# Kernel optimization log

Hardware: AMD Instinct MI355X
Metric: run time of the kernel (lower is better)

## Reference

```python
import jax, jax.numpy as jnp
import numpy as np


def _w2_1d(u, v):
    """Squared W2 distance between two 1D densities on grid positions arange(n)/n."""
    u = u / (jnp.sum(u) + 1e-10)
    v = v / (jnp.sum(v) + 1e-10)
    u_cdf = jnp.cumsum(u)                       # [n]
    v_cdf = jnp.cumsum(v)                       # [n]
    qs = jnp.sort(jnp.concatenate([u_cdf, v_cdf]))  # [2n]
    n = u.shape[0]
    pos = jnp.arange(n, dtype=u.dtype) / n      # support positions (n == m here)
    # quantile functions via searchsorted (side='left', same as torch default) + clamped gather
    u_q = pos[jnp.clip(jnp.searchsorted(u_cdf, qs), 0, n - 1)]
    v_q = pos[jnp.clip(jnp.searchsorted(v_cdf, qs), 0, n - 1)]
    delta = jnp.diff(qs, prepend=0.0)           # qs padded with leading zero, then diff
    return jnp.sum(delta * (u_q - v_q) ** 2)    # p = 2


def setup_inputs() -> dict:
    key = jax.random.key(0)
    k1, k2 = jax.random.split(key)
    B, S, T, R = 4, 8, 2048, 256
    x = jax.random.normal(k1, (B, S, T, R), dtype=jnp.float32)
    y = jax.random.normal(k2, (B, S, T, R), dtype=jnp.float32)
    return {"x": x, "y": y}


def reference(x, y):
    B, S, T, R = x.shape
    # transform_nonnegative, method='linear': shift by 1.1 * global min (if negative)
    mn = jnp.minimum(jnp.min(x), jnp.min(y))
    mn = jnp.where(mn < 0, mn, jnp.zeros((), x.dtype))
    x = x - 1.1 * mn
    y = y - 1.1 * mn
    # normalize along time axis (dim=2), sum-to-1
    x = x / jnp.sum(x, axis=2, keepdims=True)
    y = y / jnp.sum(y, axis=2, keepdims=True)
    # flatten (B, S, R) problems; each 1D distribution lives along the time axis
    xr = jnp.transpose(x, (0, 1, 3, 2)).reshape(-1, T)  # [B*S*R, T]
    yr = jnp.transpose(y, (0, 1, 3, 2)).reshape(-1, T)
    w2 = jax.vmap(_w2_1d)(xr, yr).reshape(B, S, R)
    return jnp.sum(w2, axis=(1, 2))  # loss per batch element, shape [B]
```

## Files before the change

### kernel.cpp

```cpp
#include <hip/hip_runtime.h>

#define T_N 2048
#define R_N 256
#define SLICES 32
#define NELEM (SLICES * T_N * R_N)
#define INFV 3.0e38f
#define MIN_BLOCKS 2048
#define MIN_THREADS (MIN_BLOCKS * 256)
#define LSTR 2056

#define XS(e) ((e) ^ (((e) >> 4) & 30))

#define DPPMIN(x, ctrl, rmask)                                                 \
    fminf((x), __int_as_float(__builtin_amdgcn_update_dpp(                     \
        0x7f800000, __float_as_int(x), (ctrl), (rmask), 0xf, false)))

#define DPPADDF(x, ctrl, rmask)                                                \
    x += __int_as_float(__builtin_amdgcn_update_dpp(                           \
        0, __float_as_int(x), (ctrl), (rmask), 0xf, false))

#define DPPSCAN(x)                                                             \
    do {                                                                       \
        DPPADDF(x, 0x111, 0xf);                                \
        DPPADDF(x, 0x112, 0xf);                                \
        DPPADDF(x, 0x114, 0xf);                                \
        DPPADDF(x, 0x118, 0xf);                                \
        DPPADDF(x, 0x142, 0xa);                  \
        DPPADDF(x, 0x143, 0xc);                  \
    } while (0)

__global__ __launch_bounds__(256) void kmin(const float* __restrict__ x,
                                            const float* __restrict__ y,
                                            float* __restrict__ partial,
                                            float* __restrict__ out) {
    if (blockIdx.x == 0 && threadIdx.x < 4) out[threadIdx.x] = 0.0f;
    const int g0 = blockIdx.x * 256 + threadIdx.x;
    const float4* __restrict__ x4 = (const float4*)x;
    const float4* __restrict__ y4 = (const float4*)y;
    float m0 = INFV, m1 = INFV;
    #pragma unroll
    for (int half = 0; half < 2; ++half) {
        float4 va[4], vb[4];
        #pragma unroll
        for (int it = 0; it < 4; ++it) {
            const int idx = g0 + (half * 4 + it) * MIN_THREADS;
            va[it] = x4[idx];
            vb[it] = y4[idx];
        }
        #pragma unroll
        for (int it = 0; it < 4; ++it) {
            m0 = fminf(m0, fminf(fminf(va[it].x, va[it].y), fminf(va[it].z, va[it].w)));
            m1 = fminf(m1, fminf(fminf(vb[it].x, vb[it].y), fminf(vb[it].z, vb[it].w)));
        }
    }
    float m = fminf(m0, m1);
    #pragma unroll
    for (int off = 32; off; off >>= 1) m = fminf(m, __shfl_down(m, off));
    __shared__ float sm[4];
    if ((threadIdx.x & 63) == 0) sm[threadIdx.x >> 6] = m;
    __syncthreads();
    if (threadIdx.x == 0)
        partial[blockIdx.x] = fminf(fminf(sm[0], sm[1]), fminf(sm[2], sm[3]));
}

__global__ __launch_bounds__(1024, 8) void kmain(const float* __restrict__ x,
                                                 const float* __restrict__ y,
                                                 const float* __restrict__ partial,
                                                 float* __restrict__ out) {
    __shared__ __align__(16) float L[8 * LSTR];
    __shared__ float red16[16];
    __shared__ float psum[4][2][4];
    __shared__ float pacc[4][4];

    const int tid = threadIdx.x;
    const int w = tid >> 6;
    const int lane = tid & 63;

    const int blk = blockIdx.x;
    const int xcd = blk & 7;
    const int k2 = blk >> 3;
    const int sub = k2 & 3;
    const int rest = k2 >> 2;
    const int rt = (((rest & 1) << 3) + xcd) * 4 + sub;
    const int bs = rest >> 1;
    const size_t base = (size_t)bs * (T_N * R_N) + (size_t)(rt * 4);

    const int r0 = tid << 1;
    const float4 a0 = *(const float4*)(x + base + (size_t)r0 * R_N);
    const float4 a1 = *(const float4*)(x + base + (size_t)(r0 + 1) * R_N);
    const float4 b0 = *(const float4*)(y + base + (size_t)r0 * R_N);
    const float4 b1 = *(const float4*)(y + base + (size_t)(r0 + 1) * R_N);

    {
        float m = fminf(partial[tid], partial[tid + 1024]);
        m = DPPMIN(m, 0x111, 0xf);
        m = DPPMIN(m, 0x112, 0xf);
        m = DPPMIN(m, 0x114, 0xf);
        m = DPPMIN(m, 0x118, 0xf);
        m = DPPMIN(m, 0x142, 0xa);
        m = DPPMIN(m, 0x143, 0xc);
        if (lane == 63) red16[w] = m;
    }
    if (tid < 64) L[(tid >> 3) * LSTR + T_N + (tid & 7)] = INFV;
    __syncthreads();
    float mn = red16[0];
    #pragma unroll
    for (int k = 1; k < 16; ++k) mn = fminf(mn, red16[k]);
    const float sh = 1.1f * fminf(mn, 0.0f);

    {
        const int ws_ = XS(r0);
        *(float2*)&L[0 * LSTR + ws_] = make_float2(a0.x - sh, a1.x - sh);
        *(float2*)&L[2 * LSTR + ws_] = make_float2(a0.y - sh, a1.y - sh);
        *(float2*)&L[4 * LSTR + ws_] = make_float2(a0.z - sh, a1.z - sh);
        *(float2*)&L[6 * LSTR + ws_] = make_float2(a0.w - sh, a1.w - sh);
        *(float2*)&L[1 * LSTR + ws_] = make_float2(b0.x - sh, b1.x - sh);
        *(float2*)&L[3 * LSTR + ws_] = make_float2(b0.y - sh, b1.y - sh);
        *(float2*)&L[5 * LSTR + ws_] = make_float2(b0.z - sh, b1.z - sh);
        *(float2*)&L[7 * LSTR + ws_] = make_float2(b0.w - sh, b1.w - sh);
    }
    __syncthreads();

    const int p  = w >> 2;
    const int wl = w & 3;
    const int pl = (wl << 6) | lane;
    float* __restrict__ cu = &L[(2 * p) * LSTR];
    float* __restrict__ cv = &L[(2 * p + 1) * LSTR];

    {
        int offp[4];
        #pragma unroll
        for (int c = 0; c < 4; ++c) offp[c] = XS(8 * pl + 2 * c);
        float uu[8], vv8[8];
        float su = 0.f, sv = 0.f;
        #pragma unroll
        for (int c = 0; c < 4; ++c) {
            const float2 t2 = *(const float2*)&cu[offp[c]];
            uu[2 * c] = t2.x; uu[2 * c + 1] = t2.y;
        }
        #pragma unroll
        for (int k = 0; k < 8; ++k) su += uu[k];
        #pragma unroll
        for (int c = 0; c < 4; ++c) {
            const float2 t2 = *(const float2*)&cv[offp[c]];
            vv8[2 * c] = t2.x; vv8[2 * c + 1] = t2.y;
        }
        #pragma unroll
        for (int k = 0; k < 8; ++k) sv += vv8[k];
        float iu = su, iv = sv;
        DPPSCAN(iu);
        DPPSCAN(iv);
        if (lane == 63) { psum[p][0][wl] = iu; psum[p][1][wl] = iv; }
        __syncthreads();
        float prefU = 0.f, totU = 0.f, prefV = 0.f, totV = 0.f;
        #pragma unroll
        for (int k = 0; k < 4; ++k) {
            const float a = psum[p][0][k], b = psum[p][1][k];
            totU += a; totV += b;
            if (k < wl) { prefU += a; prefV += b; }
        }
        const float invU = 1.0f / totU, invV = 1.0f / totV;
        float ru = prefU + (iu - su);
        float rv = prefV + (iv - sv);
        #pragma unroll
        for (int c = 0; c < 4; ++c) {
            const float ra = ru + uu[2 * c];
            const float rb = ra + uu[2 * c + 1];
            ru = rb;
            *(float2*)&cu[offp[c]] = make_float2(ra * invU, rb * invU);
        }
        #pragma unroll
        for (int c = 0; c < 4; ++c) {
            const float ra = rv + vv8[2 * c];
            const float rb = ra + vv8[2 * c + 1];
            rv = rb;
            *(float2*)&cv[offp[c]] = make_float2(ra * invV, rb * invV);
        }
    }
    __syncthreads();

    const int d = pl << 4;
    int i = 0, j = 0;
    if (d > 0) {
        int lo = (d > T_N) ? (d - T_N) : 0;
        int hi = (d < T_N) ? d : T_N;
        while (lo < hi) {
            const int mid = (lo + hi) >> 1;
            if (cu[XS(mid)] <= cv[XS(d - mid - 1)]) lo = mid + 1; else hi = mid;
        }
        i = lo; j = d - lo;
    }
    float qprev = 0.0f;
    if (d > 0) {
        const float pa_ = (i > 0) ? cu[XS(i - 1)] : -INFV;
        const float pb_ = (j > 0) ? cv[XS(j - 1)] : -INFV;
        qprev = fmaxf(pa_, pb_);
    }

    float uv = cu[XS(i)];
    float vv = cv[XS(j)];
    float acc = 0.0f;
    #pragma unroll
    for (int s = 0; s < 16; ++s) {
        const bool take = (uv <= vv);
        const float q = fminf(uv, vv);
        const float dd = (float)(min(i, T_N - 1) - min(j, T_N - 1));
        acc += (q - qprev) * dd * dd;
        qprev = q;
        i += take ? 1 : 0;
        j += take ? 0 : 1;
        if (s < 15) {
            const int ni = take ? i : j;
            const float* bp = take ? cu : cv;
            const float r = bp[XS(ni)];
            uv = take ? r : uv;
            vv = take ? vv : r;
        }
    }

    DPPSCAN(acc);
    if (lane == 63) pacc[p][wl] = acc;
    __syncthreads();
    if (tid == 0) {
        float r = 0.f;
        #pragma unroll
        for (int pp = 0; pp < 4; ++pp)
            r += (pacc[pp][0] + pacc[pp][1]) + (pacc[pp][2] + pacc[pp][3]);
        atomicAdd(&out[bs >> 3], r * (1.0f / ((float)T_N * (float)T_N)));
    }
}

extern "C" void kernel_launch(void* const* d_in, const int* in_sizes, int n_in,
                              void* d_out, int out_size, void* d_ws, size_t ws_size,
                              hipStream_t stream) {
    const float* x = (const float*)d_in[0];
    const float* y = (const float*)d_in[1];
    float* out = (float*)d_out;
    float* partial = (float*)d_ws;

    kmin<<<MIN_BLOCKS, 256, 0, stream>>>(x, y, partial, out);
    kmain<<<SLICES * 64, 1024, 0, stream>>>(x, y, partial, out);
}
```

Baseline: 201.3 us.

## Fuse min-reduction and W2 kernels into one persistent cooperative kernel

Replaces the two-kernel sequence (global min reduction, then the per-slice W2 computation) with a single cooperative kernel of 512 blocks. Each block first does its share of the min reduction, prefetches its first tile, and waits at a grid-wide barrier. It then loops over four work units and prefetches the next unit's data while computing the merge-path W2 on the current one. This removes a launch boundary and the second pass's startup cost, and overlaps global loads with compute. In exchange it relies on all 512 blocks being co-resident for the grid sync, runs fewer blocks in flight, and falls back to the old kernels if the cooperative launch fails.

New measurement: 281.7 us. 1.4x slower.

```diff
diff --git a/kernel.cpp b/kernel.cpp
--- a/kernel.cpp
+++ b/kernel.cpp
@@ -1,13 +1,18 @@
 #include <hip/hip_runtime.h>
+#include <hip/hip_cooperative_groups.h>
+
+namespace cg = cooperative_groups;
 
 #define T_N 2048
 #define R_N 256
 #define SLICES 32
-#define NELEM (SLICES * T_N * R_N)
 #define INFV 3.0e38f
+#define LSTR 2056
+#define GRID_B 512
+#define THR 1024
+#define TOT_THR (GRID_B * THR)
 #define MIN_BLOCKS 2048
 #define MIN_THREADS (MIN_BLOCKS * 256)
-#define LSTR 2056
 
 #define XS(e) ((e) ^ (((e) >> 4) & 30))
 
@@ -15,19 +20,242 @@
     fminf((x), __int_as_float(__builtin_amdgcn_update_dpp(                     \
         0x7f800000, __float_as_int(x), (ctrl), (rmask), 0xf, false)))
 
+#define DPPMINCHAIN(m)                                                         \
+    do {                                                                       \
+        m = DPPMIN(m, 0x111, 0xf);                                             \
+        m = DPPMIN(m, 0x112, 0xf);                                             \
+        m = DPPMIN(m, 0x114, 0xf);                                             \
+        m = DPPMIN(m, 0x118, 0xf);                                             \
+        m = DPPMIN(m, 0x142, 0xa);                                             \
+        m = DPPMIN(m, 0x143, 0xc);                                             \
+    } while (0)
+
 #define DPPADDF(x, ctrl, rmask)                                                \
     x += __int_as_float(__builtin_amdgcn_update_dpp(                           \
         0, __float_as_int(x), (ctrl), (rmask), 0xf, false))
 
 #define DPPSCAN(x)                                                             \
     do {                                                                       \
-        DPPADDF(x, 0x111, 0xf);                                \
-        DPPADDF(x, 0x112, 0xf);                                \
-        DPPADDF(x, 0x114, 0xf);                                \
-        DPPADDF(x, 0x118, 0xf);                                \
-        DPPADDF(x, 0x142, 0xa);                  \
-        DPPADDF(x, 0x143, 0xc);                  \
+        DPPADDF(x, 0x111, 0xf);                                                \
+        DPPADDF(x, 0x112, 0xf);                                                \
+        DPPADDF(x, 0x114, 0xf);                                                \
+        DPPADDF(x, 0x118, 0xf);                                                \
+        DPPADDF(x, 0x142, 0xa);                                                \
+        DPPADDF(x, 0x143, 0xc);                                                \
     } while (0)
+
+__device__ __forceinline__ size_t unit_base(int u, int* bs_out) {
+    const int xcd = u & 7;
+    const int k2 = u >> 3;
+    const int sub = k2 & 3;
+    const int rest = k2 >> 2;
+    const int rt = (((rest & 1) << 3) + xcd) * 4 + sub;
+    const int bs = rest >> 1;
+    *bs_out = bs;
+    return (size_t)bs * (T_N * R_N) + (size_t)(rt * 4);
+}
+
+__global__ __launch_bounds__(1024, 8) void kfused(const float* __restrict__ x,
+                                                  const float* __restrict__ y,
+                                                  float* __restrict__ partial,
+                                                  float* __restrict__ out) {
+    __shared__ __align__(16) float L[8 * LSTR];
+    __shared__ float red16[16];
+    __shared__ float psum[4][2][4];
+    __shared__ float pacc[4][4];
+
+    const int tid = threadIdx.x;
+    const int w = tid >> 6;
+    const int lane = tid & 63;
+    const int blk = blockIdx.x;
+
+    {
+        const int g0 = blk * THR + tid;
+        const float4* __restrict__ x4 = (const float4*)x;
+        const float4* __restrict__ y4 = (const float4*)y;
+        float m0 = INFV, m1 = INFV;
+        #pragma unroll
+        for (int half = 0; half < 2; ++half) {
+            float4 va[4], vb[4];
+            #pragma unroll
+            for (int it = 0; it < 4; ++it) {
+                const int idx = g0 + (half * 4 + it) * TOT_THR;
+                va[it] = x4[idx];
+                vb[it] = y4[idx];
+            }
+            #pragma unroll
+            for (int it = 0; it < 4; ++it) {
+                m0 = fminf(m0, fminf(fminf(va[it].x, va[it].y), fminf(va[it].z, va[it].w)));
+                m1 = fminf(m1, fminf(fminf(vb[it].x, vb[it].y), fminf(vb[it].z, vb[it].w)));
+            }
+        }
+        float m = fminf(m0, m1);
+        DPPMINCHAIN(m);
+        if (lane == 63) red16[w] = m;
+        if (blk == 0 && tid < 4) out[tid] = 0.0f;
+        __syncthreads();
+        if (tid == 0) {
+            float mm = red16[0];
+            #pragma unroll
+            for (int k = 1; k < 16; ++k) mm = fminf(mm, red16[k]);
+            partial[blk] = mm;
+        }
+    }
+
+    if (tid < 64) L[(tid >> 3) * LSTR + T_N + (tid & 7)] = INFV;
+
+    const int rr = tid << 1;
+    int bs_d;
+    const size_t b0 = unit_base(blk, &bs_d);
+    float4 pa0 = *(const float4*)(x + b0 + (size_t)rr * R_N);
+    float4 pa1 = *(const float4*)(x + b0 + (size_t)(rr + 1) * R_N);
+    float4 pb0 = *(const float4*)(y + b0 + (size_t)rr * R_N);
+    float4 pb1 = *(const float4*)(y + b0 + (size_t)(rr + 1) * R_N);
+
+    cg::this_grid().sync();
+
+    float gm = INFV;
+    #pragma unroll
+    for (int k = 0; k < 8; ++k) gm = fminf(gm, partial[lane + (k << 6)]);
+    DPPMINCHAIN(gm);
+    const float mn = __int_as_float(__builtin_amdgcn_readlane(__float_as_int(gm), 63));
+    const float sh = 1.1f * fminf(mn, 0.0f);
+
+    const int p  = w >> 2;
+    const int wl = w & 3;
+    const int pl = (wl << 6) | lane;
+    float* __restrict__ cu = &L[(2 * p) * LSTR];
+    float* __restrict__ cv = &L[(2 * p + 1) * LSTR];
+
+    #pragma unroll
+    for (int rd = 0; rd < 4; ++rd) {
+        {
+            const int ws_ = XS(rr);
+            *(float2*)&L[0 * LSTR + ws_] = make_float2(pa0.x - sh, pa1.x - sh);
+            *(float2*)&L[2 * LSTR + ws_] = make_float2(pa0.y - sh, pa1.y - sh);
+            *(float2*)&L[4 * LSTR + ws_] = make_float2(pa0.z - sh, pa1.z - sh);
+            *(float2*)&L[6 * LSTR + ws_] = make_float2(pa0.w - sh, pa1.w - sh);
+            *(float2*)&L[1 * LSTR + ws_] = make_float2(pb0.x - sh, pb1.x - sh);
+            *(float2*)&L[3 * LSTR + ws_] = make_float2(pb0.y - sh, pb1.y - sh);
+            *(float2*)&L[5 * LSTR + ws_] = make_float2(pb0.z - sh, pb1.z - sh);
+            *(float2*)&L[7 * LSTR + ws_] = make_float2(pb0.w - sh, pb1.w - sh);
+        }
+        __syncthreads();
+
+        {
+            int offp[4];
+            #pragma unroll
+            for (int c = 0; c < 4; ++c) offp[c] = XS(8 * pl + 2 * c);
+            float uu[8], vv8[8];
+            float su = 0.f, sv = 0.f;
+            #pragma unroll
+            for (int c = 0; c < 4; ++c) {
+                const float2 t2 = *(const float2*)&cu[offp[c]];
+                uu[2 * c] = t2.x; uu[2 * c + 1] = t2.y;
+            }
+            #pragma unroll
+            for (int k = 0; k < 8; ++k) su += uu[k];
+            #pragma unroll
+            for (int c = 0; c < 4; ++c) {
+                const float2 t2 = *(const float2*)&cv[offp[c]];
+                vv8[2 * c] = t2.x; vv8[2 * c + 1] = t2.y;
+            }
+            #pragma unroll
+            for (int k = 0; k < 8; ++k) sv += vv8[k];
+            float iu = su, iv = sv;
+            DPPSCAN(iu);
+            DPPSCAN(iv);
+            if (lane == 63) { psum[p][0][wl] = iu; psum[p][1][wl] = iv; }
+            __syncthreads();
+            float prefU = 0.f, totU = 0.f, prefV = 0.f, totV = 0.f;
+            #pragma unroll
+            for (int k = 0; k < 4; ++k) {
+                const float a = psum[p][0][k], b = psum[p][1][k];
+                totU += a; totV += b;
+                if (k < wl) { prefU += a; prefV += b; }
+            }
+            const float invU = 1.0f / totU, invV = 1.0f / totV;
+            float ru = prefU + (iu - su);
+            float rv = prefV + (iv - sv);
+            #pragma unroll
+            for (int c = 0; c < 4; ++c) {
+                const float ra = ru + uu[2 * c];
+                const float rb = ra + uu[2 * c + 1];
+                ru = rb;
+                *(float2*)&cu[offp[c]] = make_float2(ra * invU, rb * invU);
+            }
+            #pragma unroll
+            for (int c = 0; c < 4; ++c) {
+                const float ra = rv + vv8[2 * c];
+                const float rb = ra + vv8[2 * c + 1];
+                rv = rb;
+                *(float2*)&cv[offp[c]] = make_float2(ra * invV, rb * invV);
+            }
+        }
+        __syncthreads();
+
+        if (rd < 3) {
+            int bs_n;
+            const size_t bn = unit_base(((rd + 1) << 9) | blk, &bs_n);
+            pa0 = *(const float4*)(x + bn + (size_t)rr * R_N);
+            pa1 = *(const float4*)(x + bn + (size_t)(rr + 1) * R_N);
+            pb0 = *(const float4*)(y + bn + (size_t)rr * R_N);
+            pb1 = *(const float4*)(y + bn + (size_t)(rr + 1) * R_N);
+        }
+
+        const int d = pl << 4;
+        int i = 0, j = 0;
+        if (d > 0) {
+            int lo = (d > T_N) ? (d - T_N) : 0;
+            int hi = (d < T_N) ? d : T_N;
+            while (lo < hi) {
+                const int mid = (lo + hi) >> 1;
+                if (cu[XS(mid)] <= cv[XS(d - mid - 1)]) lo = mid + 1; else hi = mid;
+            }
+            i = lo; j = d - lo;
+        }
+        float qprev = 0.0f;
+        if (d > 0) {
+            const float pa_ = (i > 0) ? cu[XS(i - 1)] : -INFV;
+            const float pb_ = (j > 0) ? cv[XS(j - 1)] : -INFV;
+            qprev = fmaxf(pa_, pb_);
+        }
+
+        float uv = cu[XS(i)];
+        float vv = cv[XS(j)];
+        float acc = 0.0f;
+        #pragma unroll
+        for (int s = 0; s < 16; ++s) {
+            const bool take = (uv <= vv);
+            const float q = fminf(uv, vv);
+            const float dd = (float)(min(i, T_N - 1) - min(j, T_N - 1));
+            acc += (q - qprev) * dd * dd;
+            qprev = q;
+            i += take ? 1 : 0;
+            j += take ? 0 : 1;
+            if (s < 15) {
+                const int ni = take ? i : j;
+                const float* bp = take ? cu : cv;
+                const float rf = bp[XS(ni)];
+                uv = take ? rf : uv;
+                vv = take ? vv : rf;
+            }
+        }
+
+        DPPSCAN(acc);
+        if (lane == 63) pacc[p][wl] = acc;
+        __syncthreads();
+        if (tid == 0) {
+            float rsum = 0.f;
+            #pragma unroll
+            for (int pp = 0; pp < 4; ++pp)
+                rsum += (pacc[pp][0] + pacc[pp][1]) + (pacc[pp][2] + pacc[pp][3]);
+            int bs_r;
+            unit_base((rd << 9) | blk, &bs_r);
+            atomicAdd(&out[bs_r >> 3], rsum * (1.0f / ((float)T_N * (float)T_N)));
+        }
+    }
+}
 
 __global__ __launch_bounds__(256) void kmin(const float* __restrict__ x,
                                             const float* __restrict__ y,
@@ -77,13 +305,9 @@
     const int lane = tid & 63;
 
     const int blk = blockIdx.x;
-    const int xcd = blk & 7;
-    const int k2 = blk >> 3;
-    const int sub = k2 & 3;
-    const int rest = k2 >> 2;
-    const int rt = (((rest & 1) << 3) + xcd) * 4 + sub;
-    const int bs = rest >> 1;
-    const size_t base = (size_t)bs * (T_N * R_N) + (size_t)(rt * 4);
+    int bs_;
+    const size_t base = unit_base(blk, &bs_);
+    const int bs = bs_;
 
     const int r0 = tid << 1;
     const float4 a0 = *(const float4*)(x + base + (size_t)r0 * R_N);
@@ -93,12 +317,7 @@
 
     {
         float m = fminf(partial[tid], partial[tid + 1024]);
-        m = DPPMIN(m, 0x111, 0xf);
-        m = DPPMIN(m, 0x112, 0xf);
-        m = DPPMIN(m, 0x114, 0xf);
-        m = DPPMIN(m, 0x118, 0xf);
-        m = DPPMIN(m, 0x142, 0xa);
-        m = DPPMIN(m, 0x143, 0xc);
+        DPPMINCHAIN(m);
         if (lane == 63) red16[w] = m;
     }
     if (tid < 64) L[(tid >> 3) * LSTR + T_N + (tid & 7)] = INFV;
@@ -212,9 +431,9 @@
         if (s < 15) {
             const int ni = take ? i : j;
             const float* bp = take ? cu : cv;
-            const float r = bp[XS(ni)];
-            uv = take ? r : uv;
-            vv = take ? vv : r;
+            const float rf = bp[XS(ni)];
+            uv = take ? rf : uv;
+            vv = take ? vv : rf;
         }
     }
 
@@ -222,11 +441,11 @@
     if (lane == 63) pacc[p][wl] = acc;
     __syncthreads();
     if (tid == 0) {
-        float r = 0.f;
+        float rsum = 0.f;
         #pragma unroll
         for (int pp = 0; pp < 4; ++pp)
-            r += (pacc[pp][0] + pacc[pp][1]) + (pacc[pp][2] + pacc[pp][3]);
-        atomicAdd(&out[bs >> 3], r * (1.0f / ((float)T_N * (float)T_N)));
+            rsum += (pacc[pp][0] + pacc[pp][1]) + (pacc[pp][2] + pacc[pp][3]);
+        atomicAdd(&out[bs >> 3], rsum * (1.0f / ((float)T_N * (float)T_N)));
     }
 }
 
@@ -238,6 +457,11 @@
     float* out = (float*)d_out;
     float* partial = (float*)d_ws;
 
-    kmin<<<MIN_BLOCKS, 256, 0, stream>>>(x, y, partial, out);
-    kmain<<<SLICES * 64, 1024, 0, stream>>>(x, y, partial, out);
+    void* args[] = {(void*)&x, (void*)&y, (void*)&partial, (void*)&out};
+    const hipError_t e = hipLaunchCooperativeKernel(
+        (const void*)kfused, dim3(GRID_B), dim3(THR), args, 0, stream);
+    if (e != hipSuccess) {
+        kmin<<<MIN_BLOCKS, 256, 0, stream>>>(x, y, partial, out);
+        kmain<<<SLICES * 64, 1024, 0, stream>>>(x, y, partial, out);
+    }
 }
```
